# Kernel optimization log

Measured on AMD Instinct MI355X. Metric: run time of the kernel, lower is better.

## Reference

```python
import jax, jax.numpy as jnp
import numpy as np

SCALE = 0.08838834764831845  # head_dim ** -0.5
NUM_HEADS = 32
NUM_KV_HEADS = 8
HEAD_DIM = 128
PAGE_SIZE = 16


def setup_inputs() -> dict:
    key = jax.random.key(0)
    k1, k2 = jax.random.split(key)
    B = 32
    L0_PAGES = 256        # shared prefix: 4096 tokens
    L1_PAGES = 64         # per-seq chunk: 1024 tokens
    L2_PAGES = 32         # per-seq suffix: 512 tokens
    P = L0_PAGES + B * L1_PAGES + B * L2_PAGES  # 3328 pages
    q = jax.random.normal(k1, (B, NUM_HEADS * HEAD_DIM), jnp.float32)
    # paged KV cache, layout [page, k/v, page_size, kv_heads, head_dim]
    kv_cache = jax.random.normal(k2, (P, 2, PAGE_SIZE, NUM_KV_HEADS, HEAD_DIM), jnp.float32)
    shared_page_idx = jnp.arange(L0_PAGES, dtype=jnp.int32)
    seq1_page_idx = (L0_PAGES + jnp.arange(B * L1_PAGES, dtype=jnp.int32)).reshape(B, L1_PAGES)
    seq2_page_idx = (L0_PAGES + B * L1_PAGES + jnp.arange(B * L2_PAGES, dtype=jnp.int32)).reshape(B, L2_PAGES)
    return {"q": q, "kv_cache": kv_cache, "shared_page_idx": shared_page_idx,
            "seq1_page_idx": seq1_page_idx, "seq2_page_idx": seq2_page_idx}


def _softmax_attn(scores, V, av_eq):
    # scores: [..., L]; returns (out, lse) with a single stable pass
    m = scores.max(axis=-1, keepdims=True)
    e = jnp.exp(scores - m)
    denom = e.sum(axis=-1)
    out = jnp.einsum(av_eq, e, V) / denom[..., None]
    lse = m[..., 0] + jnp.log(denom)
    return out, lse


def _merge_state(oa, sa, ob, sb):
    # flashinfer.merge_state: LSE-weighted combination of attention states
    s = jnp.logaddexp(sa, sb)
    o = oa * jnp.exp(sa - s)[..., None] + ob * jnp.exp(sb - s)[..., None]
    return o, s


def _forward(q, kv_cache, shared_page_idx, seq1_page_idx, seq2_page_idx):
    B = q.shape[0]
    G = NUM_HEADS // NUM_KV_HEADS  # GQA group size = 4
    # q -> [B, Hkv, G, D]
    q4 = q.reshape(B, NUM_KV_HEADS, G, HEAD_DIM)

    # level 0: shared pages -> [L0, Hkv, D]
    K0 = kv_cache[shared_page_idx, 0].reshape(-1, NUM_KV_HEADS, HEAD_DIM)
    V0 = kv_cache[shared_page_idx, 1].reshape(-1, NUM_KV_HEADS, HEAD_DIM)
    s0 = jnp.einsum('bkgd,lkd->bkgl', q4, K0) * SCALE
    out, lse = _softmax_attn(s0, V0, 'bkgl,lkd->bkgd')

    # levels 1 and 2: per-sequence paged KV -> [B, Li, Hkv, D]
    for idx in (seq1_page_idx, seq2_page_idx):
        Ki = kv_cache[idx, 0].reshape(B, -1, NUM_KV_HEADS, HEAD_DIM)
        Vi = kv_cache[idx, 1].reshape(B, -1, NUM_KV_HEADS, HEAD_DIM)
        si = jnp.einsum('bkgd,blkd->bkgl', q4, Ki) * SCALE
        oi, li = _softmax_attn(si, Vi, 'bkgl,blkd->bkgd')
        out, lse = _merge_state(out, lse, oi, li)

    return out.reshape(B, NUM_HEADS * HEAD_DIM)


def reference(q, kv_cache, shared_page_idx, seq1_page_idx, seq2_page_idx):
    return _forward(q, kv_cache, shared_page_idx, seq1_page_idx, seq2_page_idx)
```

## Files before the change

### kernel.cpp

```cpp
#include <hip/hip_runtime.h>
#include <stdint.h>


namespace {
constexpr int kG = 4, kD = 128;
constexpr float kQS = 0.08838834764831845f * 1.4426950408889634f;
constexpr int kNChunk = 64;
constexpr int kNTile = 24;
constexpr int kNSrc = kNChunk + kNTile;
constexpr size_t kOParts = (size_t)kNSrc * 32 * 8 * 4 * 128;
constexpr size_t kMLB = kOParts;
constexpr size_t kWsFloats = kOParts + (size_t)kNSrc * 32 * 8 * 4 * 2;
}

__device__ __forceinline__ float wave_max(float v) {
#pragma unroll
    for (int off = 1; off < 64; off <<= 1) v = fmaxf(v, __shfl_xor(v, off));
    return v;
}
__device__ __forceinline__ float wave_sum(float v) {
#pragma unroll
    for (int off = 1; off < 64; off <<= 1) v += __shfl_xor(v, off);
    return v;
}
__device__ __forceinline__ int kslot(int s, int t) { return s ^ (t & 31); }
__device__ __forceinline__ int vslot(int s, int t) {
    return s ^ (((t << 1) & 31) | ((t >> 4) & 1));
}
__device__ __forceinline__ void gll16(const float* gp, float* lp) {
    __builtin_amdgcn_global_load_lds(
        (const __attribute__((address_space(1))) void*)gp,
        (__attribute__((address_space(3))) void*)lp, 16, 0, 0);
}

__global__ __launch_bounds__(512, 2)
void fused_kernel(const float* __restrict__ q, const float* __restrict__ kv,
                  const int* __restrict__ sp0, const int* __restrict__ sp1,
                  const int* __restrict__ sp2, float* __restrict__ ws)
{
    __shared__ __align__(16) float smem[16384];
    __shared__ int pgs[4];

    const int bid = blockIdx.x;
    const int tid = threadIdx.x;
    const int w = tid >> 6, lane = tid & 63;
    const int ts = lane >> 4, dg = lane & 15;
    const int l0id = bid / 13;

    if (bid % 13 == 0) {
        const int h = l0id & 7, c4 = l0id >> 3;
        if (tid < 4) pgs[tid] = sp0[c4 * 4 + tid];
        __syncthreads();
        {
            const int t = tid >> 3;
            const int sg = (tid & 7) * 4;
            const int pg = pgs[t >> 4];
            const float* gk = kv + (size_t)pg * 32768u + (size_t)(t & 15) * 1024u + h * 128;
#pragma unroll
            for (int j = 0; j < 4; ++j) {
                const int s = sg + j;
                *(float4*)&smem[t * 128 + (kslot(s, t) << 2)] =
                    *(const float4*)(gk + s * 4);
                *(float4*)&smem[8192 + t * 128 + (vslot(s, t) << 2)] =
                    *(const float4*)(gk + 16384 + s * 4);
            }
        }
        __syncthreads();

        const int wq = __builtin_amdgcn_readfirstlane(w);
        for (int pass = 0; pass < 4; ++pass) {
            const int b = wq * 4 + pass;
            const float* qb = q + (size_t)b * 4096 + h * 512;
            float s[4] = {0.f, 0.f, 0.f, 0.f};
#pragma unroll
            for (int c = 0; c < 16; ++c) {
                float4 ka = *(const float4*)&smem[lane * 128 + (kslot(2 * c, lane) << 2)];
                float4 kb = *(const float4*)&smem[lane * 128 + (kslot(2 * c + 1, lane) << 2)];
#pragma unroll
                for (int g = 0; g < 4; ++g) {
                    float4 qa = *(const float4*)(qb + g * 128 + c * 8);
                    float4 q2 = *(const float4*)(qb + g * 128 + c * 8 + 4);
                    s[g] += ka.x * qa.x + ka.y * qa.y + ka.z * qa.z + ka.w * qa.w
                          + kb.x * q2.x + kb.y * q2.y + kb.z * q2.z + kb.w * q2.w;
                }
            }
            float m[4], p[4], l[4], acc[4][8];
#pragma unroll
            for (int g = 0; g < 4; ++g) {
                s[g] *= kQS;
                m[g] = wave_max(s[g]);
                p[g] = exp2f(s[g] - m[g]);
                l[g] = wave_sum(p[g]);
#pragma unroll
                for (int e = 0; e < 8; ++e) acc[g][e] = 0.f;
            }
#pragma unroll
            for (int j = 0; j < 16; ++j) {
                const int t = ts * 16 + j;
                float4 va = *(const float4*)&smem[8192 + t * 128 + (vslot(2 * dg, t) << 2)];
                float4 vb = *(const float4*)&smem[8192 + t * 128 + (vslot(2 * dg + 1, t) << 2)];
#pragma unroll
                for (int g = 0; g < 4; ++g) {
                    float pj = __shfl(p[g], t);
                    acc[g][0] = fmaf(pj, va.x, acc[g][0]);
                    acc[g][1] = fmaf(pj, va.y, acc[g][1]);
                    acc[g][2] = fmaf(pj, va.z, acc[g][2]);
                    acc[g][3] = fmaf(pj, va.w, acc[g][3]);
                    acc[g][4] = fmaf(pj, vb.x, acc[g][4]);
                    acc[g][5] = fmaf(pj, vb.y, acc[g][5]);
                    acc[g][6] = fmaf(pj, vb.z, acc[g][6]);
                    acc[g][7] = fmaf(pj, vb.w, acc[g][7]);
                }
            }
#pragma unroll
            for (int g = 0; g < 4; ++g)
#pragma unroll
                for (int e = 0; e < 8; ++e) {
                    float v = acc[g][e];
                    v += __shfl_xor(v, 16);
                    v += __shfl_xor(v, 32);
                    acc[g][e] = v;
                }
            if (lane < 16) {
                const size_t ob = ((((size_t)c4 * 32 + b) * 8 + h) * 4) * 128 + lane * 8;
#pragma unroll
                for (int g = 0; g < 4; ++g) {
                    *(float4*)&ws[ob + (size_t)g * 128] =
                        make_float4(acc[g][0], acc[g][1], acc[g][2], acc[g][3]);
                    *(float4*)&ws[ob + (size_t)g * 128 + 4] =
                        make_float4(acc[g][4], acc[g][5], acc[g][6], acc[g][7]);
                }
            }
            if (lane == 0) {
                const size_t idx = (((size_t)c4 * 32 + b) * 8 + h) * 4;
#pragma unroll
                for (int g = 0; g < 4; ++g) {
                    ws[kMLB + 2 * (idx + g)] = m[g];
                    ws[kMLB + 2 * (idx + g) + 1] = l[g];
                }
            }
        }
    } else {
        const int sid = bid - l0id - 1;
        const int b = sid / 192;
        const int h = (sid / 24) & 7;
        const int tle = sid % 24;
        const int wq = __builtin_amdgcn_readfirstlane(w);

        const int jw = tle * 4 + (wq >> 1);
        const int pgw = (jw < 64) ? sp1[b * 64 + jw] : sp2[b * 32 + (jw - 64)];
        const size_t poff = (size_t)pgw * 32768u;

        {
            const int sl = lane & 31;
            const int rl = lane >> 5;
#pragma unroll
            for (int i = 0; i < 4; ++i) {
                const int r = wq * 8 + i * 2 + rl;
                const float* gk = kv + poff + (size_t)(r & 15) * 1024u + h * 128;
                gll16(gk + ((sl ^ (r & 31)) << 2),
                      &smem[wq * 1024 + i * 256]);
                const int vm = ((r << 1) & 31) | ((r >> 4) & 1);
                gll16(gk + 16384 + ((sl ^ vm) << 2),
                      &smem[8192 + wq * 1024 + i * 256]);
            }
        }
        __syncthreads();

        if (wq < 4) {
            const int g = wq;
            const float* qb = q + (size_t)b * 4096 + h * 512 + g * 128;
            float s = 0.f;
#pragma unroll
            for (int c = 0; c < 16; ++c) {
                float4 ka = *(const float4*)&smem[lane * 128 + (kslot(2 * c, lane) << 2)];
                float4 kb = *(const float4*)&smem[lane * 128 + (kslot(2 * c + 1, lane) << 2)];
                float4 qa = *(const float4*)(qb + c * 8);
                float4 q2 = *(const float4*)(qb + c * 8 + 4);
                s += ka.x * qa.x + ka.y * qa.y + ka.z * qa.z + ka.w * qa.w
                   + kb.x * q2.x + kb.y * q2.y + kb.z * q2.z + kb.w * q2.w;
            }
            s *= kQS;
            const float m = wave_max(s);
            const float p = exp2f(s - m);
            const float l = wave_sum(p);
            float acc[8];
#pragma unroll
            for (int e = 0; e < 8; ++e) acc[e] = 0.f;
#pragma unroll
            for (int j = 0; j < 16; ++j) {
                const int t = ts * 16 + j;
                float4 va = *(const float4*)&smem[8192 + t * 128 + (vslot(2 * dg, t) << 2)];
                float4 vb = *(const float4*)&smem[8192 + t * 128 + (vslot(2 * dg + 1, t) << 2)];
                const float pj = __shfl(p, t);
                acc[0] = fmaf(pj, va.x, acc[0]);
                acc[1] = fmaf(pj, va.y, acc[1]);
                acc[2] = fmaf(pj, va.z, acc[2]);
                acc[3] = fmaf(pj, va.w, acc[3]);
                acc[4] = fmaf(pj, vb.x, acc[4]);
                acc[5] = fmaf(pj, vb.y, acc[5]);
                acc[6] = fmaf(pj, vb.z, acc[6]);
                acc[7] = fmaf(pj, vb.w, acc[7]);
            }
#pragma unroll
            for (int e = 0; e < 8; ++e) {
                float v = acc[e];
                v += __shfl_xor(v, 16);
                v += __shfl_xor(v, 32);
                acc[e] = v;
            }
            const size_t src = (size_t)(kNChunk + tle);
            if (lane < 16) {
                const size_t ob = (((src * 32 + b) * 8 + h) * 4 + g) * 128 + lane * 8;
                *(float4*)&ws[ob]     = make_float4(acc[0], acc[1], acc[2], acc[3]);
                *(float4*)&ws[ob + 4] = make_float4(acc[4], acc[5], acc[6], acc[7]);
            }
            if (lane == 0) {
                const size_t idx = ((src * 32 + b) * 8 + h) * 4 + g;
                ws[kMLB + 2 * idx] = m;
                ws[kMLB + 2 * idx + 1] = l;
            }
        }
    }
}

__global__ __launch_bounds__(128, 8)
void merge_kernel(const float* __restrict__ ws, float* __restrict__ out)
{
    __shared__ float sm[kNSrc], sls[kNSrc], sc[kNSrc];
    const int bid = blockIdx.x;
    const int b = bid >> 5, h = (bid >> 2) & 7, g = bid & 3;
    const int tid = threadIdx.x;
    if (tid < kNSrc) {
        const size_t idx = (((size_t)tid * 32 + b) * 8 + h) * 4 + g;
        sm[tid]  = ws[kMLB + 2 * idx];
        sls[tid] = ws[kMLB + 2 * idx + 1];
    }
    __syncthreads();
    float mstar = -1e30f;
#pragma unroll
    for (int s = 0; s < kNSrc; ++s) mstar = fmaxf(mstar, sm[s]);
    if (tid < kNSrc) sc[tid] = exp2f(sm[tid] - mstar);
    __syncthreads();
    float denom = 0.f;
#pragma unroll
    for (int s = 0; s < kNSrc; ++s) denom = fmaf(sc[s], sls[s], denom);
    const size_t base = ((((size_t)b * 8 + h) * 4 + g) * 128) + tid;
    float numer = 0.f;
#pragma unroll 1
    for (int s0 = 0; s0 < kNSrc; s0 += 8) {
        float v[8];
#pragma unroll
        for (int k = 0; k < 8; ++k)
            v[k] = ws[base + (size_t)(s0 + k) * 131072u];
#pragma unroll
        for (int k = 0; k < 8; ++k)
            numer = fmaf(sc[s0 + k], v[k], numer);
    }
    out[(size_t)b * 4096 + h * 512 + g * 128 + tid] = numer / denom;
}

__global__ __launch_bounds__(512, 2)
void fallback_kernel(const float* __restrict__ q, const float* __restrict__ kv,
                     const int* __restrict__ sp0, const int* __restrict__ sp1,
                     const int* __restrict__ sp2, float* __restrict__ out)
{
    __shared__ __align__(16) float qs[kG * kD];
    __shared__ int plist[352];
    __shared__ __align__(16) float wacc[8][kG * kD];
    __shared__ float wm[8][kG], wl[8][kG];
    const int b = blockIdx.x >> 3, h = blockIdx.x & 7;
    const int tid = threadIdx.x;
    {
        const int g = tid >> 7, d = tid & 127;
        qs[g * 128 + d] = q[(size_t)b * 4096 + h * 512 + g * 128 + d] * kQS;
    }
    if (tid < 352) {
        int pg;
        if (tid < 256)      pg = sp0[tid];
        else if (tid < 320) pg = sp1[b * 64 + (tid - 256)];
        else                pg = sp2[b * 32 + (tid - 320)];
        plist[tid] = pg;
    }
    __syncthreads();
    const int w = tid >> 6, lane = tid & 63;
    const int ts = lane >> 4, dg = lane & 15;
    const float4* qv4 = (const float4*)qs;
    float m[kG], l[kG], acc[kG][8];
#pragma unroll
    for (int g = 0; g < kG; ++g) {
        m[g] = -1e30f; l[g] = 0.f;
#pragma unroll
        for (int e = 0; e < 8; ++e) acc[g][e] = 0.f;
    }
    for (int tile = 0; tile < 11; ++tile) {
        const int page = plist[w * 44 + tile * 4 + ts];
        const size_t poff = (size_t)page * 32768u;
        const float* Kp = kv + poff + (size_t)(lane & 15) * 1024u + h * 128;
        const float* Vp = kv + poff + 16384u + h * 128 + dg * 8;
        float s[kG] = {0.f, 0.f, 0.f, 0.f};
#pragma unroll
        for (int c = 0; c < 16; ++c) {
            float4 ka = *(const float4*)(Kp + c * 8);
            float4 kb = *(const float4*)(Kp + c * 8 + 4);
#pragma unroll
            for (int g = 0; g < kG; ++g) {
                float4 qa = qv4[g * 32 + c * 2];
                float4 qb = qv4[g * 32 + c * 2 + 1];
                s[g] += ka.x * qa.x + ka.y * qa.y + ka.z * qa.z + ka.w * qa.w
                      + kb.x * qb.x + kb.y * qb.y + kb.z * qb.z + kb.w * qb.w;
            }
        }
        float p[kG];
#pragma unroll
        for (int g = 0; g < kG; ++g) {
            float mt = wave_max(s[g]);
            float mn = fmaxf(m[g], mt);
            float alpha = exp2f(m[g] - mn);
            p[g] = exp2f(s[g] - mn);
            m[g] = mn;
            l[g] = l[g] * alpha + wave_sum(p[g]);
#pragma unroll
            for (int e = 0; e < 8; ++e) acc[g][e] *= alpha;
        }
#pragma unroll
        for (int j = 0; j < 16; ++j) {
            const int t = ts * 16 + j;
            float4 va = *(const float4*)(Vp + (size_t)j * 1024u);
            float4 vb = *(const float4*)(Vp + (size_t)j * 1024u + 4);
#pragma unroll
            for (int g = 0; g < kG; ++g) {
                float pj = __shfl(p[g], t);
                acc[g][0] = fmaf(pj, va.x, acc[g][0]);
                acc[g][1] = fmaf(pj, va.y, acc[g][1]);
                acc[g][2] = fmaf(pj, va.z, acc[g][2]);
                acc[g][3] = fmaf(pj, va.w, acc[g][3]);
                acc[g][4] = fmaf(pj, vb.x, acc[g][4]);
                acc[g][5] = fmaf(pj, vb.y, acc[g][5]);
                acc[g][6] = fmaf(pj, vb.z, acc[g][6]);
                acc[g][7] = fmaf(pj, vb.w, acc[g][7]);
            }
        }
    }
#pragma unroll
    for (int g = 0; g < kG; ++g)
#pragma unroll
        for (int e = 0; e < 8; ++e) {
            float v = acc[g][e];
            v += __shfl_xor(v, 16);
            v += __shfl_xor(v, 32);
            acc[g][e] = v;
        }
    if (lane < 16) {
#pragma unroll
        for (int g = 0; g < kG; ++g) {
            *(float4*)&wacc[w][g * 128 + dg * 8]     = make_float4(acc[g][0], acc[g][1], acc[g][2], acc[g][3]);
            *(float4*)&wacc[w][g * 128 + dg * 8 + 4] = make_float4(acc[g][4], acc[g][5], acc[g][6], acc[g][7]);
        }
        if (lane == 0)
#pragma unroll
            for (int g = 0; g < kG; ++g) { wm[w][g] = m[g]; wl[w][g] = l[g]; }
    }
    __syncthreads();
    {
        const int g = tid >> 7, d = tid & 127;
        float mstar = wm[0][g];
#pragma unroll
        for (int ww = 1; ww < 8; ++ww) mstar = fmaxf(mstar, wm[ww][g]);
        float numer = 0.f, denom = 0.f;
#pragma unroll
        for (int ww = 0; ww < 8; ++ww) {
            float sc = exp2f(wm[ww][g] - mstar);
            denom = fmaf(sc, wl[ww][g], denom);
            numer = fmaf(sc, wacc[ww][g * 128 + d], numer);
        }
        out[(size_t)b * 4096 + h * 512 + g * 128 + d] = numer / denom;
    }
}

extern "C" void kernel_launch(void* const* d_in, const int* in_sizes, int n_in,
                              void* d_out, int out_size, void* d_ws, size_t ws_size,
                              hipStream_t stream) {
    const float* q  = (const float*)d_in[0];
    const float* kv = (const float*)d_in[1];
    const int* sp0 = (const int*)d_in[2];
    const int* sp1 = (const int*)d_in[3];
    const int* sp2 = (const int*)d_in[4];
    float* out = (float*)d_out;
    float* ws = (float*)d_ws;
    if (ws_size >= kWsFloats * sizeof(float)) {
        hipLaunchKernelGGL(fused_kernel, dim3(6656), dim3(512), 0, stream,
                           q, kv, sp0, sp1, sp2, ws);
        hipLaunchKernelGGL(merge_kernel, dim3(1024), dim3(128), 0, stream, ws, out);
    } else {
        hipLaunchKernelGGL(fallback_kernel, dim3(256), dim3(512), 0, stream,
                           q, kv, sp0, sp1, sp2, out);
    }
}
```

Measured before the change: 819.0 us.

## Split fused attention kernel into shared-prefix and per-sequence kernels with register-streamed KV

Splits the fused kernel into two launches: one for the shared-prefix level and a new seq_kernel for the per-sequence pages. The new kernel drops the LDS staging and the wave that sat idle in the old per-sequence path. Each wave instead loads K and V directly from global memory into registers, double-buffered so the next loads overlap the FMAs, and handles all four GQA heads per wave. This is meant to remove LDS traffic, the block-wide barrier and wasted warps in the memory-bound per-sequence phase. The cost is one more kernel launch, less overlap between the two levels, and higher register pressure.

```diff
diff --git a/kernel.cpp b/kernel.cpp
--- a/kernel.cpp
+++ b/kernel.cpp
@@ -27,199 +27,235 @@
 __device__ __forceinline__ int vslot(int s, int t) {
     return s ^ (((t << 1) & 31) | ((t >> 4) & 1));
 }
-__device__ __forceinline__ void gll16(const float* gp, float* lp) {
-    __builtin_amdgcn_global_load_lds(
-        (const __attribute__((address_space(1))) void*)gp,
-        (__attribute__((address_space(3))) void*)lp, 16, 0, 0);
-}
 
 __global__ __launch_bounds__(512, 2)
-void fused_kernel(const float* __restrict__ q, const float* __restrict__ kv,
-                  const int* __restrict__ sp0, const int* __restrict__ sp1,
-                  const int* __restrict__ sp2, float* __restrict__ ws)
+void l0_kernel(const float* __restrict__ q, const float* __restrict__ kv,
+               const int* __restrict__ sp0, float* __restrict__ ws)
 {
     __shared__ __align__(16) float smem[16384];
     __shared__ int pgs[4];
 
     const int bid = blockIdx.x;
+    const int h = bid & 7, c4 = bid >> 3;
     const int tid = threadIdx.x;
     const int w = tid >> 6, lane = tid & 63;
     const int ts = lane >> 4, dg = lane & 15;
-    const int l0id = bid / 13;
-
-    if (bid % 13 == 0) {
-        const int h = l0id & 7, c4 = l0id >> 3;
-        if (tid < 4) pgs[tid] = sp0[c4 * 4 + tid];
-        __syncthreads();
-        {
-            const int t = tid >> 3;
-            const int sg = (tid & 7) * 4;
-            const int pg = pgs[t >> 4];
-            const float* gk = kv + (size_t)pg * 32768u + (size_t)(t & 15) * 1024u + h * 128;
-#pragma unroll
-            for (int j = 0; j < 4; ++j) {
-                const int s = sg + j;
-                *(float4*)&smem[t * 128 + (kslot(s, t) << 2)] =
-                    *(const float4*)(gk + s * 4);
-                *(float4*)&smem[8192 + t * 128 + (vslot(s, t) << 2)] =
-                    *(const float4*)(gk + 16384 + s * 4);
-            }
-        }
-        __syncthreads();
-
-        const int wq = __builtin_amdgcn_readfirstlane(w);
-        for (int pass = 0; pass < 4; ++pass) {
-            const int b = wq * 4 + pass;
-            const float* qb = q + (size_t)b * 4096 + h * 512;
-            float s[4] = {0.f, 0.f, 0.f, 0.f};
-#pragma unroll
-            for (int c = 0; c < 16; ++c) {
-                float4 ka = *(const float4*)&smem[lane * 128 + (kslot(2 * c, lane) << 2)];
-                float4 kb = *(const float4*)&smem[lane * 128 + (kslot(2 * c + 1, lane) << 2)];
-#pragma unroll
-                for (int g = 0; g < 4; ++g) {
-                    float4 qa = *(const float4*)(qb + g * 128 + c * 8);
-                    float4 q2 = *(const float4*)(qb + g * 128 + c * 8 + 4);
-                    s[g] += ka.x * qa.x + ka.y * qa.y + ka.z * qa.z + ka.w * qa.w
-                          + kb.x * q2.x + kb.y * q2.y + kb.z * q2.z + kb.w * q2.w;
-                }
-            }
-            float m[4], p[4], l[4], acc[4][8];
+
+    if (tid < 4) pgs[tid] = sp0[c4 * 4 + tid];
+    __syncthreads();
+    {
+        const int t = tid >> 3;
+        const int sg = (tid & 7) * 4;
+        const int pg = pgs[t >> 4];
+        const float* gk = kv + (size_t)pg * 32768u + (size_t)(t & 15) * 1024u + h * 128;
+#pragma unroll
+        for (int j = 0; j < 4; ++j) {
+            const int s = sg + j;
+            *(float4*)&smem[t * 128 + (kslot(s, t) << 2)] =
+                *(const float4*)(gk + s * 4);
+            *(float4*)&smem[8192 + t * 128 + (vslot(s, t) << 2)] =
+                *(const float4*)(gk + 16384 + s * 4);
+        }
+    }
+    __syncthreads();
+
+    const int wq = __builtin_amdgcn_readfirstlane(w);
+    for (int pass = 0; pass < 4; ++pass) {
+        const int b = wq * 4 + pass;
+        const float* qb = q + (size_t)b * 4096 + h * 512;
+        float s[4] = {0.f, 0.f, 0.f, 0.f};
+#pragma unroll
+        for (int c = 0; c < 16; ++c) {
+            float4 ka = *(const float4*)&smem[lane * 128 + (kslot(2 * c, lane) << 2)];
+            float4 kb = *(const float4*)&smem[lane * 128 + (kslot(2 * c + 1, lane) << 2)];
 #pragma unroll
             for (int g = 0; g < 4; ++g) {
-                s[g] *= kQS;
-                m[g] = wave_max(s[g]);
-                p[g] = exp2f(s[g] - m[g]);
-                l[g] = wave_sum(p[g]);
-#pragma unroll
-                for (int e = 0; e < 8; ++e) acc[g][e] = 0.f;
-            }
-#pragma unroll
-            for (int j = 0; j < 16; ++j) {
-                const int t = ts * 16 + j;
-                float4 va = *(const float4*)&smem[8192 + t * 128 + (vslot(2 * dg, t) << 2)];
-                float4 vb = *(const float4*)&smem[8192 + t * 128 + (vslot(2 * dg + 1, t) << 2)];
-#pragma unroll
-                for (int g = 0; g < 4; ++g) {
-                    float pj = __shfl(p[g], t);
-                    acc[g][0] = fmaf(pj, va.x, acc[g][0]);
-                    acc[g][1] = fmaf(pj, va.y, acc[g][1]);
-                    acc[g][2] = fmaf(pj, va.z, acc[g][2]);
-                    acc[g][3] = fmaf(pj, va.w, acc[g][3]);
-                    acc[g][4] = fmaf(pj, vb.x, acc[g][4]);
-                    acc[g][5] = fmaf(pj, vb.y, acc[g][5]);
-                    acc[g][6] = fmaf(pj, vb.z, acc[g][6]);
-                    acc[g][7] = fmaf(pj, vb.w, acc[g][7]);
-                }
-            }
-#pragma unroll
-            for (int g = 0; g < 4; ++g)
-#pragma unroll
-                for (int e = 0; e < 8; ++e) {
-                    float v = acc[g][e];
-                    v += __shfl_xor(v, 16);
-                    v += __shfl_xor(v, 32);
-                    acc[g][e] = v;
-                }
-            if (lane < 16) {
-                const size_t ob = ((((size_t)c4 * 32 + b) * 8 + h) * 4) * 128 + lane * 8;
-#pragma unroll
-                for (int g = 0; g < 4; ++g) {
-                    *(float4*)&ws[ob + (size_t)g * 128] =
-                        make_float4(acc[g][0], acc[g][1], acc[g][2], acc[g][3]);
-                    *(float4*)&ws[ob + (size_t)g * 128 + 4] =
-                        make_float4(acc[g][4], acc[g][5], acc[g][6], acc[g][7]);
-                }
-            }
-            if (lane == 0) {
-                const size_t idx = (((size_t)c4 * 32 + b) * 8 + h) * 4;
-#pragma unroll
-                for (int g = 0; g < 4; ++g) {
-                    ws[kMLB + 2 * (idx + g)] = m[g];
-                    ws[kMLB + 2 * (idx + g) + 1] = l[g];
-                }
-            }
-        }
-    } else {
-        const int sid = bid - l0id - 1;
-        const int b = sid / 192;
-        const int h = (sid / 24) & 7;
-        const int tle = sid % 24;
-        const int wq = __builtin_amdgcn_readfirstlane(w);
-
-        const int jw = tle * 4 + (wq >> 1);
-        const int pgw = (jw < 64) ? sp1[b * 64 + jw] : sp2[b * 32 + (jw - 64)];
-        const size_t poff = (size_t)pgw * 32768u;
-
-        {
-            const int sl = lane & 31;
-            const int rl = lane >> 5;
-#pragma unroll
-            for (int i = 0; i < 4; ++i) {
-                const int r = wq * 8 + i * 2 + rl;
-                const float* gk = kv + poff + (size_t)(r & 15) * 1024u + h * 128;
-                gll16(gk + ((sl ^ (r & 31)) << 2),
-                      &smem[wq * 1024 + i * 256]);
-                const int vm = ((r << 1) & 31) | ((r >> 4) & 1);
-                gll16(gk + 16384 + ((sl ^ vm) << 2),
-                      &smem[8192 + wq * 1024 + i * 256]);
-            }
-        }
-        __syncthreads();
-
-        if (wq < 4) {
-            const int g = wq;
-            const float* qb = q + (size_t)b * 4096 + h * 512 + g * 128;
-            float s = 0.f;
-#pragma unroll
-            for (int c = 0; c < 16; ++c) {
-                float4 ka = *(const float4*)&smem[lane * 128 + (kslot(2 * c, lane) << 2)];
-                float4 kb = *(const float4*)&smem[lane * 128 + (kslot(2 * c + 1, lane) << 2)];
-                float4 qa = *(const float4*)(qb + c * 8);
-                float4 q2 = *(const float4*)(qb + c * 8 + 4);
-                s += ka.x * qa.x + ka.y * qa.y + ka.z * qa.z + ka.w * qa.w
-                   + kb.x * q2.x + kb.y * q2.y + kb.z * q2.z + kb.w * q2.w;
-            }
-            s *= kQS;
-            const float m = wave_max(s);
-            const float p = exp2f(s - m);
-            const float l = wave_sum(p);
-            float acc[8];
-#pragma unroll
-            for (int e = 0; e < 8; ++e) acc[e] = 0.f;
-#pragma unroll
-            for (int j = 0; j < 16; ++j) {
-                const int t = ts * 16 + j;
-                float4 va = *(const float4*)&smem[8192 + t * 128 + (vslot(2 * dg, t) << 2)];
-                float4 vb = *(const float4*)&smem[8192 + t * 128 + (vslot(2 * dg + 1, t) << 2)];
-                const float pj = __shfl(p, t);
-                acc[0] = fmaf(pj, va.x, acc[0]);
-                acc[1] = fmaf(pj, va.y, acc[1]);
-                acc[2] = fmaf(pj, va.z, acc[2]);
-                acc[3] = fmaf(pj, va.w, acc[3]);
-                acc[4] = fmaf(pj, vb.x, acc[4]);
-                acc[5] = fmaf(pj, vb.y, acc[5]);
-                acc[6] = fmaf(pj, vb.z, acc[6]);
-                acc[7] = fmaf(pj, vb.w, acc[7]);
-            }
+                float4 qa = *(const float4*)(qb + g * 128 + c * 8);
+                float4 q2 = *(const float4*)(qb + g * 128 + c * 8 + 4);
+                s[g] += ka.x * qa.x + ka.y * qa.y + ka.z * qa.z + ka.w * qa.w
+                      + kb.x * q2.x + kb.y * q2.y + kb.z * q2.z + kb.w * q2.w;
+            }
+        }
+        float m[4], p[4], l[4], acc[4][8];
+#pragma unroll
+        for (int g = 0; g < 4; ++g) {
+            s[g] *= kQS;
+            m[g] = wave_max(s[g]);
+            p[g] = exp2f(s[g] - m[g]);
+            l[g] = wave_sum(p[g]);
+#pragma unroll
+            for (int e = 0; e < 8; ++e) acc[g][e] = 0.f;
+        }
+#pragma unroll
+        for (int j = 0; j < 16; ++j) {
+            const int t = ts * 16 + j;
+            float4 va = *(const float4*)&smem[8192 + t * 128 + (vslot(2 * dg, t) << 2)];
+            float4 vb = *(const float4*)&smem[8192 + t * 128 + (vslot(2 * dg + 1, t) << 2)];
+#pragma unroll
+            for (int g = 0; g < 4; ++g) {
+                float pj = __shfl(p[g], t);
+                acc[g][0] = fmaf(pj, va.x, acc[g][0]);
+                acc[g][1] = fmaf(pj, va.y, acc[g][1]);
+                acc[g][2] = fmaf(pj, va.z, acc[g][2]);
+                acc[g][3] = fmaf(pj, va.w, acc[g][3]);
+                acc[g][4] = fmaf(pj, vb.x, acc[g][4]);
+                acc[g][5] = fmaf(pj, vb.y, acc[g][5]);
+                acc[g][6] = fmaf(pj, vb.z, acc[g][6]);
+                acc[g][7] = fmaf(pj, vb.w, acc[g][7]);
+            }
+        }
+#pragma unroll
+        for (int g = 0; g < 4; ++g)
 #pragma unroll
             for (int e = 0; e < 8; ++e) {
-                float v = acc[e];
+                float v = acc[g][e];
                 v += __shfl_xor(v, 16);
                 v += __shfl_xor(v, 32);
-                acc[e] = v;
-            }
-            const size_t src = (size_t)(kNChunk + tle);
-            if (lane < 16) {
-                const size_t ob = (((src * 32 + b) * 8 + h) * 4 + g) * 128 + lane * 8;
-                *(float4*)&ws[ob]     = make_float4(acc[0], acc[1], acc[2], acc[3]);
-                *(float4*)&ws[ob + 4] = make_float4(acc[4], acc[5], acc[6], acc[7]);
-            }
-            if (lane == 0) {
-                const size_t idx = ((src * 32 + b) * 8 + h) * 4 + g;
-                ws[kMLB + 2 * idx] = m;
-                ws[kMLB + 2 * idx + 1] = l;
-            }
+                acc[g][e] = v;
+            }
+        if (lane < 16) {
+            const size_t ob = ((((size_t)c4 * 32 + b) * 8 + h) * 4) * 128 + lane * 8;
+#pragma unroll
+            for (int g = 0; g < 4; ++g) {
+                *(float4*)&ws[ob + (size_t)g * 128] =
+                    make_float4(acc[g][0], acc[g][1], acc[g][2], acc[g][3]);
+                *(float4*)&ws[ob + (size_t)g * 128 + 4] =
+                    make_float4(acc[g][4], acc[g][5], acc[g][6], acc[g][7]);
+            }
+        }
+        if (lane == 0) {
+            const size_t idx = (((size_t)c4 * 32 + b) * 8 + h) * 4;
+#pragma unroll
+            for (int g = 0; g < 4; ++g) {
+                ws[kMLB + 2 * (idx + g)] = m[g];
+                ws[kMLB + 2 * (idx + g) + 1] = l[g];
+            }
+        }
+    }
+}
+
+#define K_LOAD(dst, off)                                                    \
+    _Pragma("unroll")                                                       \
+    for (int i = 0; i < 8; ++i) dst[i] = Kp[(off) + i];
+#define K_FMA(cur, BB)                                                      \
+    _Pragma("unroll")                                                       \
+    for (int i = 0; i < 8; ++i) {                                           \
+        float4 kk = cur[i];                                                 \
+        _Pragma("unroll")                                                   \
+        for (int g = 0; g < 4; ++g) {                                       \
+            float4 qq = qv4[g * 32 + (BB) * 8 + i];                         \
+            s[g] += kk.x * qq.x + kk.y * qq.y + kk.z * qq.z + kk.w * qq.w;  \
+        }                                                                   \
+    }
+#define V_LOAD(dst, j0)                                                     \
+    _Pragma("unroll")                                                       \
+    for (int j = 0; j < 4; ++j) {                                           \
+        dst[2 * j]     = Vp[((j0) + j) * 256];                              \
+        dst[2 * j + 1] = Vp[((j0) + j) * 256 + 1];                          \
+    }
+#define V_FMA(cur, JB)                                                     \
+    _Pragma("unroll")                                                       \
+    for (int jj = 0; jj < 4; ++jj) {                                        \
+        const int t = ts * 16 + (JB) * 4 + jj;                              \
+        float4 x = cur[2 * jj], y = cur[2 * jj + 1];                        \
+        _Pragma("unroll")                                                   \
+        for (int g = 0; g < 4; ++g) {                                       \
+            float pj = __shfl(p[g], t);                                     \
+            acc[g][0] = fmaf(pj, x.x, acc[g][0]);                           \
+            acc[g][1] = fmaf(pj, x.y, acc[g][1]);                           \
+            acc[g][2] = fmaf(pj, x.z, acc[g][2]);                           \
+            acc[g][3] = fmaf(pj, x.w, acc[g][3]);                           \
+            acc[g][4] = fmaf(pj, y.x, acc[g][4]);                           \
+            acc[g][5] = fmaf(pj, y.y, acc[g][5]);                           \
+            acc[g][6] = fmaf(pj, y.z, acc[g][6]);                           \
+            acc[g][7] = fmaf(pj, y.w, acc[g][7]);                           \
+        }                                                                   \
+    }
+
+__global__ __launch_bounds__(256, 4)
+void seq_kernel(const float* __restrict__ q, const float* __restrict__ kv,
+                const int* __restrict__ sp1, const int* __restrict__ sp2,
+                float* __restrict__ ws)
+{
+    const int tid = threadIdx.x;
+    const int w = tid >> 6, lane = tid & 63;
+    const int ts = lane >> 4, dg = lane & 15;
+    const int bid = blockIdx.x;
+    const int b  = bid / 48;
+    const int h  = (bid / 6) & 7;
+    const int tg = bid % 6;
+    const int tile = tg * 4 + __builtin_amdgcn_readfirstlane(w);
+
+    const int jw = tile * 4 + ts;
+    const int pg = (jw < 64) ? sp1[b * 64 + jw] : sp2[b * 32 + (jw - 64)];
+    const size_t poff = (size_t)pg * 32768u;
+
+    const float4* Kp  = (const float4*)(kv + poff + (size_t)(lane & 15) * 1024u + (size_t)h * 128);
+    const float4* qv4 = (const float4*)(q + (size_t)b * 4096 + (size_t)h * 512);
+
+    float4 kb0[8], kb1[8];
+    float s[4] = {0.f, 0.f, 0.f, 0.f};
+    K_LOAD(kb0, 0)
+    K_LOAD(kb1, 8)
+    K_FMA(kb0, 0)
+    K_LOAD(kb0, 16)
+    K_FMA(kb1, 1)
+    K_LOAD(kb1, 24)
+    K_FMA(kb0, 2)
+    K_FMA(kb1, 3)
+
+    const float4* Vp = (const float4*)(kv + poff + 16384u + (size_t)h * 128 + dg * 8);
+    float4 v0[8], v1[8];
+    V_LOAD(v0, 0)
+
+    float m[4], p[4], l[4];
+#pragma unroll
+    for (int g = 0; g < 4; ++g) {
+        s[g] *= kQS;
+        m[g] = wave_max(s[g]);
+        p[g] = exp2f(s[g] - m[g]);
+        l[g] = wave_sum(p[g]);
+    }
+    float acc[4][8];
+#pragma unroll
+    for (int g = 0; g < 4; ++g)
+#pragma unroll
+        for (int e = 0; e < 8; ++e) acc[g][e] = 0.f;
+
+    V_LOAD(v1, 4)
+    V_FMA(v0, 0)
+    V_LOAD(v0, 8)
+    V_FMA(v1, 1)
+    V_LOAD(v1, 12)
+    V_FMA(v0, 2)
+    V_FMA(v1, 3)
+
+#pragma unroll
+    for (int g = 0; g < 4; ++g)
+#pragma unroll
+        for (int e = 0; e < 8; ++e) {
+            float v = acc[g][e];
+            v += __shfl_xor(v, 16);
+            v += __shfl_xor(v, 32);
+            acc[g][e] = v;
+        }
+    const size_t src = (size_t)(kNChunk + tile);
+    if (lane < 16) {
+        const size_t ob = (((src * 32 + b) * 8 + h) * 4) * 128 + lane * 8;
+#pragma unroll
+        for (int g = 0; g < 4; ++g) {
+            *(float4*)&ws[ob + (size_t)g * 128] =
+                make_float4(acc[g][0], acc[g][1], acc[g][2], acc[g][3]);
+            *(float4*)&ws[ob + (size_t)g * 128 + 4] =
+                make_float4(acc[g][4], acc[g][5], acc[g][6], acc[g][7]);
+        }
+    }
+    if (lane == 0) {
+        const size_t idx = ((src * 32 + b) * 8 + h) * 4;
+#pragma unroll
+        for (int g = 0; g < 4; ++g) {
+            ws[kMLB + 2 * (idx + g)] = m[g];
+            ws[kMLB + 2 * (idx + g) + 1] = l[g];
         }
     }
 }
@@ -389,8 +425,8 @@
     float* out = (float*)d_out;
     float* ws = (float*)d_ws;
     if (ws_size >= kWsFloats * sizeof(float)) {
-        hipLaunchKernelGGL(fused_kernel, dim3(6656), dim3(512), 0, stream,
-                           q, kv, sp0, sp1, sp2, ws);
+        hipLaunchKernelGGL(l0_kernel,    dim3(512),  dim3(512), 0, stream, q, kv, sp0, ws);
+        hipLaunchKernelGGL(seq_kernel,   dim3(1536), dim3(256), 0, stream, q, kv, sp1, sp2, ws);
         hipLaunchKernelGGL(merge_kernel, dim3(1024), dim3(128), 0, stream, ws, out);
     } else {
         hipLaunchKernelGGL(fallback_kernel, dim3(256), dim3(512), 0, stream,
```

Measured after the change: 780.5 us. -4.7%, faster.
